# Kernel optimization log

Measured on AMD Instinct MI355X. Metric: run time of the kernel, lower is better.

Reference implementation:

```python
import jax, jax.numpy as jnp
import numpy as np

B, N, M, E, H = 8, 4096, 4, 512, 8
HEAD_DIM = E // H
LN_EPS = 1e-5


def setup_inputs() -> dict:
    key = jax.random.key(0)
    ks = jax.random.split(key, 12)
    inp = {}
    for i in range(M):
        inp[f"f{i}"] = jax.random.normal(ks[i], (B, N, E), dtype=jnp.float32)
    # learned query (flattened from [1,1,E])
    inp["q_param"] = jax.random.normal(ks[4], (E,), dtype=jnp.float32)
    # torch nn.MultiheadAttention packed in-projection [3E, E] and bias [3E]
    inp["in_proj_w"] = jax.random.normal(ks[5], (3 * E, E), dtype=jnp.float32) * 0.02
    inp["in_proj_b"] = jnp.zeros((3 * E,), dtype=jnp.float32)
    inp["out_proj_w"] = jax.random.normal(ks[6], (E, E), dtype=jnp.float32) * 0.02
    inp["out_proj_b"] = jnp.zeros((E,), dtype=jnp.float32)
    inp["ln_gamma"] = jnp.ones((E,), dtype=jnp.float32)
    inp["ln_beta"] = jnp.zeros((E,), dtype=jnp.float32)
    return inp


def reference(f0, f1, f2, f3, q_param, in_proj_w, in_proj_b, out_proj_w, out_proj_b, ln_gamma, ln_beta):
    x = jnp.stack([f0, f1, f2, f3], axis=2)  # [B, N, M, E]
    b, n, m, e = x.shape
    h, d = H, e // H
    scale = 1.0 / np.sqrt(d)

    Wq, Wk, Wv = jnp.split(in_proj_w, 3, axis=0)  # each [E, E]
    bq, bk, bv = jnp.split(in_proj_b, 3)

    # single learned query, shared across all (b, n) instances
    qh = ((Wq @ q_param + bq) * scale).reshape(h, d)  # [H, d]

    k = (jnp.einsum('bnme,fe->bnmf', x, Wk) + bk).reshape(b, n, m, h, d)
    v = (jnp.einsum('bnme,fe->bnmf', x, Wv) + bv).reshape(b, n, m, h, d)

    scores = jnp.einsum('hd,bnmhd->bnhm', qh, k)        # [B, N, H, M]
    attn = jax.nn.softmax(scores, axis=-1)
    o = jnp.einsum('bnhm,bnmhd->bnhd', attn, v).reshape(b, n, e)
    o = o @ out_proj_w.T + out_proj_b                   # [B, N, E]

    mu = jnp.mean(o, axis=-1, keepdims=True)
    var = jnp.var(o, axis=-1, keepdims=True)
    return (o - mu) * jax.lax.rsqrt(var + LN_EPS) * ln_gamma + ln_beta
```

## Files before the change

### kernel.cpp

```cpp
#include <hip/hip_runtime.h>
#include <hip/hip_bf16.h>


typedef float  f32x4  __attribute__((ext_vector_type(4)));
typedef float  f32x16 __attribute__((ext_vector_type(16)));
typedef short  short8 __attribute__((ext_vector_type(8)));

typedef __attribute__((address_space(1))) const void GV;
typedef __attribute__((address_space(3))) void LV;

__device__ __forceinline__ unsigned short f2bf(float f) {
  unsigned int x = __float_as_uint(f);
  unsigned int r = (x + 0x7fffu + ((x >> 16) & 1u)) >> 16;
  return (unsigned short)r;
}

__device__ __forceinline__ short8 pack8(const f32x4& a, const f32x4& b) {
  unsigned int r0, r1, r2, r3;
  asm("v_cvt_pk_bf16_f32 %0, %1, %2" : "=v"(r0) : "v"(a[0]), "v"(a[1]));
  asm("v_cvt_pk_bf16_f32 %0, %1, %2" : "=v"(r1) : "v"(a[2]), "v"(a[3]));
  asm("v_cvt_pk_bf16_f32 %0, %1, %2" : "=v"(r2) : "v"(b[0]), "v"(b[1]));
  asm("v_cvt_pk_bf16_f32 %0, %1, %2" : "=v"(r3) : "v"(b[2]), "v"(b[3]));
  short8 r;
  r[0] = (short)(r0 & 0xffff); r[1] = (short)(r0 >> 16);
  r[2] = (short)(r1 & 0xffff); r[3] = (short)(r1 >> 16);
  r[4] = (short)(r2 & 0xffff); r[5] = (short)(r2 >> 16);
  r[6] = (short)(r3 & 0xffff); r[7] = (short)(r3 >> 16);
  return r;
}

__device__ __forceinline__ void mfma32(f32x16& c, short8 a, short8 b) {
  asm("v_mfma_f32_32x32x16_bf16 %0, %1, %2, %0" : "+v"(c) : "v"(a), "v"(b));
}
__device__ __forceinline__ void mfma16(f32x4& c, short8 a, short8 b) {
  asm("v_mfma_f32_16x16x32_bf16 %0, %1, %2, %0" : "+v"(c) : "v"(a), "v"(b));
}

__device__ __forceinline__ void gld4s(short8& d, const unsigned short* p) {
  asm volatile("global_load_dwordx4 %0, %1, off" : "=v"(d) : "v"(p));
}

#define WAITV(n) asm volatile("s_waitcnt vmcnt(" #n ")" ::: "memory")

__device__ __forceinline__ void wbv12(short8& a, short8& b, short8& c, short8& d,
                                      short8& e, short8& f, short8& g, short8& h) {
  asm volatile("s_waitcnt vmcnt(12)"
               : "+v"(a), "+v"(b), "+v"(c), "+v"(d),
                 "+v"(e), "+v"(f), "+v"(g), "+v"(h));
}
__device__ __forceinline__ void wbv8(short8& a, short8& b, short8& c, short8& d,
                                     short8& e, short8& f, short8& g, short8& h) {
  asm volatile("s_waitcnt vmcnt(8)"
               : "+v"(a), "+v"(b), "+v"(c), "+v"(d),
                 "+v"(e), "+v"(f), "+v"(g), "+v"(h));
}
__device__ __forceinline__ void wbv0(short8& a, short8& b, short8& c, short8& d,
                                     short8& e, short8& f, short8& g, short8& h) {
  asm volatile("s_waitcnt vmcnt(0)"
               : "+v"(a), "+v"(b), "+v"(c), "+v"(d),
                 "+v"(e), "+v"(f), "+v"(g), "+v"(h));
}

__global__ void __launch_bounds__(512) tdcp_k0(
    const float* __restrict__ q_param, const float* __restrict__ in_w,
    const float* __restrict__ in_b, const float* __restrict__ out_w,
    float* __restrict__ scoreb, unsigned short* __restrict__ wscB,
    unsigned short* __restrict__ WvB, unsigned short* __restrict__ WoB)
{
  const int tid = threadIdx.x;
  const int blk = blockIdx.x;
  if (blk < 8) {
    const int h = blk;
    __shared__ float qls[512];
    __shared__ float qs[64];
    qls[tid] = q_param[tid];
    __syncthreads();
    {
      const int io = tid >> 3, sub = tid & 7;
      const float* wrow = in_w + (size_t)(h * 64 + io) * 512;
      float v = 0.f;
      #pragma unroll 8
      for (int ee = 0; ee < 64; ++ee) {
        const int e = sub + (ee << 3);
        v += wrow[e] * qls[e];
      }
      v += __shfl_xor(v, 1); v += __shfl_xor(v, 2); v += __shfl_xor(v, 4);
      if (sub == 0) qs[io] = (v + in_b[h * 64 + io]) * 0.125f;
    }
    __syncthreads();
    {
      const int e = tid;
      const float* wk = in_w + (size_t)(512 + h * 64) * 512 + e;
      float v = 0.f;
      #pragma unroll 8
      for (int jj = 0; jj < 64; ++jj) v += qs[jj] * wk[jj * 512];
      const int s32 = e >> 5, g = (e & 31) >> 3, j = e & 7;
      wscB[((s32 << 6) + h + (g << 4)) * 8 + j] = f2bf(v);
      wscB[((s32 << 6) + (h + 8) + (g << 4)) * 8 + j] = 0;
    }
    if (tid < 64) {
      float v = qs[tid] * in_b[512 + h * 64 + tid];
      v += __shfl_xor(v, 1);  v += __shfl_xor(v, 2);  v += __shfl_xor(v, 4);
      v += __shfl_xor(v, 8);  v += __shfl_xor(v, 16); v += __shfl_xor(v, 32);
      if (tid == 0) scoreb[h] = v;
    }
    if (blk == 0 && tid >= 64 && tid < 72) scoreb[tid - 56] = 0.f;
  } else {
    const int mb = blk - 8;
    const bool isWo = mb >= 64;
    const float* src = isWo ? out_w : (in_w + (size_t)1024 * 512);
    unsigned short* dst = isWo ? WoB : WvB;
    const int slot = ((mb & 63) << 9) + tid;
    const int ct = slot >> 11, kt = (slot >> 6) & 31, ln = slot & 63;
    const float* p = src + (size_t)(ct * 32 + (ln & 31)) * 512
                         + kt * 16 + ((ln >> 5) << 3);
    const f32x4 u0 = *(const f32x4*)(p);
    const f32x4 u1 = *(const f32x4*)(p + 4);
    short8 rr;
    rr[0] = (short)f2bf(u0[0]); rr[1] = (short)f2bf(u0[1]);
    rr[2] = (short)f2bf(u0[2]); rr[3] = (short)f2bf(u0[3]);
    rr[4] = (short)f2bf(u1[0]); rr[5] = (short)f2bf(u1[1]);
    rr[6] = (short)f2bf(u1[2]); rr[7] = (short)f2bf(u1[3]);
    *(short8*)(dst + slot * 8) = rr;
  }
}

__global__ void __launch_bounds__(512, 2) tdcp_k1(
    const float* __restrict__ f0, const float* __restrict__ f1,
    const float* __restrict__ f2, const float* __restrict__ f3,
    const float* __restrict__ in_b,
    const float* __restrict__ scoreb, const unsigned short* __restrict__ wscB,
    const unsigned short* __restrict__ WvB, const unsigned short* __restrict__ WoB,
    const float* __restrict__ out_b, const float* __restrict__ gamma,
    const float* __restrict__ beta, float* __restrict__ out)
{
  extern __shared__ __align__(16) char smem[];
  const int tid = threadIdx.x;
  const int w = tid >> 6;
  const int l = tid & 63;
  const int tok0 = blockIdx.x << 5;

  {
    const f32x4* wsrc = (const f32x4*)wscB;
    f32x4* wdst = (f32x4*)(smem + 98304);
    wdst[tid * 2] = wsrc[tid * 2];
    wdst[tid * 2 + 1] = wsrc[tid * 2 + 1];
  }

  const float* gsrc[4];
  #pragma unroll
  for (int q = 0; q < 4; ++q) {
    const int R = 16 * w + 4 * q + (l >> 4);
    const int m = R & 3, tok = R >> 2;
    const int u = (((l & 15) >> 1) ^ (R & 7));
    gsrc[q] = (m == 0 ? f0 : m == 1 ? f1 : m == 2 ? f2 : f3)
              + (size_t)(tok0 + tok) * 512 + (u << 3) + ((l & 1) << 2);
  }
  const int dmaDst = (w << 12);

  const int aB = (l & 31) << 8;
  int offA[4];
  #pragma unroll
  for (int kt4 = 0; kt4 < 4; ++kt4)
    offA[kt4] = (((2 * kt4 + (l >> 5)) ^ (l & 7)) << 5);
  const int sB = (16 * w + (l & 15)) << 8;
  int offS[2];
  #pragma unroll
  for (int sc = 0; sc < 2; ++sc)
    offS[sc] = (((4 * sc + (l >> 4)) ^ (l & 7)) << 5);

  const int ct0 = w << 1;
  const unsigned short* wv0 = WvB + (((ct0 * 32) << 6) + l) * 8;
  const unsigned short* wv1 = WvB + ((((ct0 + 1) * 32) << 6) + l) * 8;
  const unsigned short* wscL = (const unsigned short*)(smem + 98304);

  f32x16 acc[4][2];
  f32x4 sacc;
  #pragma unroll
  for (int i = 0; i < 4; ++i)
    #pragma unroll
    for (int cc = 0; cc < 2; ++cc)
      #pragma unroll
      for (int r = 0; r < 16; ++r) acc[i][cc][r] = 0.f;
  sacc[0] = sacc[1] = sacc[2] = sacc[3] = 0.f;

  short8 bb[2][8];

#define DMA(S) do { \
    char* db_ = smem + 32768 * ((S) % 3) + dmaDst; \
    __builtin_amdgcn_global_load_lds((GV*)(gsrc[0] + (S) * 64), (LV*)(db_),        16, 0, 0); \
    __builtin_amdgcn_global_load_lds((GV*)(gsrc[1] + (S) * 64), (LV*)(db_ + 1024), 16, 0, 0); \
    __builtin_amdgcn_global_load_lds((GV*)(gsrc[2] + (S) * 64), (LV*)(db_ + 2048), 16, 0, 0); \
    __builtin_amdgcn_global_load_lds((GV*)(gsrc[3] + (S) * 64), (LV*)(db_ + 3072), 16, 0, 0); \
  } while (0)

#define ISSUE_B(S, bank) do { \
    gld4s(bb[bank][0], wv0 + ((S) * 4 + 0) * 512); \
    gld4s(bb[bank][1], wv1 + ((S) * 4 + 0) * 512); \
    gld4s(bb[bank][2], wv0 + ((S) * 4 + 1) * 512); \
    gld4s(bb[bank][3], wv1 + ((S) * 4 + 1) * 512); \
    gld4s(bb[bank][4], wv0 + ((S) * 4 + 2) * 512); \
    gld4s(bb[bank][5], wv1 + ((S) * 4 + 2) * 512); \
    gld4s(bb[bank][6], wv0 + ((S) * 4 + 3) * 512); \
    gld4s(bb[bank][7], wv1 + ((S) * 4 + 3) * 512); \
  } while (0)

  DMA(0); DMA(1);
  ISSUE_B(0, 0);
  WAITV(12);
  asm volatile("s_waitcnt lgkmcnt(0)" ::: "memory");
  __builtin_amdgcn_s_barrier();
  asm volatile("" ::: "memory");

  #pragma unroll
  for (int s = 0; s < 8; ++s) {
    if (s < 6) DMA(s + 2);
    if (s < 7) ISSUE_B(s + 1, (s + 1) & 1);

    short8 (&b)[8] = bb[s & 1];
    if (s < 6)      wbv12(b[0], b[1], b[2], b[3], b[4], b[5], b[6], b[7]);
    else if (s == 6) wbv8(b[0], b[1], b[2], b[3], b[4], b[5], b[6], b[7]);
    else             wbv0(b[0], b[1], b[2], b[3], b[4], b[5], b[6], b[7]);

    const char* cur = smem + 32768 * (s % 3);
    const short8 sb0 = *(const short8*)(wscL + (((2 * s) << 6) + l) * 8);
    const short8 sb1 = *(const short8*)(wscL + (((2 * s + 1) << 6) + l) * 8);
    #pragma unroll
    for (int kt4 = 0; kt4 < 4; ++kt4) {
      #pragma unroll
      for (int rt = 0; rt < 4; ++rt) {
        const char* p = cur + (rt << 13) + aB + offA[kt4];
        const f32x4 lo = *(const f32x4*)(p);
        const f32x4 hi = *(const f32x4*)(p + 16);
        const short8 a = pack8(lo, hi);
        mfma32(acc[rt][0], a, b[kt4 * 2]);
        mfma32(acc[rt][1], a, b[kt4 * 2 + 1]);
      }
      if ((kt4 & 1) == 0) {
        const int sc = kt4 >> 1;
        const char* p = cur + sB + offS[sc];
        const f32x4 lo = *(const f32x4*)(p);
        const f32x4 hi = *(const f32x4*)(p + 16);
        mfma16(sacc, pack8(lo, hi), (sc == 0) ? sb0 : sb1);
      }
    }

    if (s < 6)      { WAITV(12); }
    else if (s == 6) { WAITV(8); }
    if (s < 7) {
      asm volatile("s_waitcnt lgkmcnt(0)" ::: "memory");
      __builtin_amdgcn_s_barrier();
      asm volatile("" ::: "memory");
    }
  }
  asm volatile("s_nop 7\n\ts_nop 7\n\ts_nop 7" ::);

  {
    const int hh = l & 15;
    if (hh < 8) {
      const float sb = scoreb[hh];
      const float s0 = sacc[0] + sb, s1 = sacc[1] + sb;
      const float s2 = sacc[2] + sb, s3 = sacc[3] + sb;
      const float mx = fmaxf(fmaxf(s0, s1), fmaxf(s2, s3));
      const float e0 = __expf(s0 - mx), e1 = __expf(s1 - mx);
      const float e2 = __expf(s2 - mx), e3 = __expf(s3 - mx);
      const float inv = 1.f / (e0 + e1 + e2 + e3);
      f32x4 av; av[0] = e0 * inv; av[1] = e1 * inv; av[2] = e2 * inv; av[3] = e3 * inv;
      const int t = (w << 2) + (l >> 4);
      *(f32x4*)(smem + 65536 + (((t << 3) + hh) << 4)) = av;
    }
  }
  __syncthreads();

  {
    unsigned short* omid = (unsigned short*)(smem);
    #pragma unroll
    for (int c2 = 0; c2 < 2; ++c2) {
      const int ff = ((ct0 + c2) << 5) + (l & 31);
      const float bvf = in_b[1024 + ff];
      const int ktf = ff >> 4;
      const int laneL = ((l >> 3) & 1) << 5;
      const int elem = ff & 7;
      #pragma unroll
      for (int rt = 0; rt < 4; ++rt) {
        #pragma unroll
        for (int tt = 0; tt < 4; ++tt) {
          const int t = (rt << 3) + (tt << 1) + (l >> 5);
          const f32x4 av = *(const f32x4*)(smem + 65536 + (((t << 3) + w) << 4));
          const float o = av[0] * acc[rt][c2][tt * 4 + 0]
                        + av[1] * acc[rt][c2][tt * 4 + 1]
                        + av[2] * acc[rt][c2][tt * 4 + 2]
                        + av[3] * acc[rt][c2][tt * 4 + 3] + bvf;
          omid[((ktf << 6) + t + laneL) * 8 + elem] = f2bf(o);
        }
      }
    }
  }
  __syncthreads();

  f32x16 oa0, oa1;
  #pragma unroll
  for (int r = 0; r < 16; ++r) { oa0[r] = 0.f; oa1[r] = 0.f; }
  const unsigned short* wo0 = WoB + (((ct0 * 32) << 6) + l) * 8;
  const unsigned short* wo1 = WoB + ((((ct0 + 1) * 32) << 6) + l) * 8;
  const int a_off = l << 4;
  #pragma unroll 4
  for (int kt = 0; kt < 32; ++kt) {
    const short8 a = *(const short8*)(smem + (kt << 10) + a_off);
    mfma32(oa0, a, *(const short8*)(wo0 + kt * 512));
    mfma32(oa1, a, *(const short8*)(wo1 + kt * 512));
  }
  asm volatile("s_nop 7\n\ts_nop 7\n\ts_nop 7" ::);

  {
    const int g0 = (ct0 << 5) + (l & 31);
    const int g1 = g0 + 32;
    const float ob0 = out_b[g0], ob1 = out_b[g1];
    const float gm0 = gamma[g0], gm1 = gamma[g1];
    const float bt0 = beta[g0],  bt1 = beta[g1];
    float* stats = (float*)(smem + 69632);
    #pragma unroll
    for (int r = 0; r < 16; ++r) {
      const float v0 = oa0[r] + ob0, v1 = oa1[r] + ob1;
      float s = v0 + v1, qq = v0 * v0 + v1 * v1;
      s += __shfl_xor(s, 16); qq += __shfl_xor(qq, 16);
      s += __shfl_xor(s, 8);  qq += __shfl_xor(qq, 8);
      s += __shfl_xor(s, 4);  qq += __shfl_xor(qq, 4);
      s += __shfl_xor(s, 2);  qq += __shfl_xor(qq, 2);
      s += __shfl_xor(s, 1);  qq += __shfl_xor(qq, 1);
      if ((l & 31) == 0) {
        const int t = (r & 3) + ((r >> 2) << 3) + ((l >> 5) << 2);
        stats[(t << 4) + (w << 1)] = s;
        stats[(t << 4) + (w << 1) + 1] = qq;
      }
    }
    __syncthreads();
    #pragma unroll
    for (int r = 0; r < 16; ++r) {
      const int t = (r & 3) + ((r >> 2) << 3) + ((l >> 5) << 2);
      const float* st = stats + (t << 4);
      float s = 0.f, qq = 0.f;
      #pragma unroll
      for (int ww = 0; ww < 8; ++ww) { s += st[2 * ww]; qq += st[2 * ww + 1]; }
      const float mu = s * 0.001953125f;
      const float rs = rsqrtf(qq * 0.001953125f - mu * mu + 1e-5f);
      const float v0 = oa0[r] + ob0, v1 = oa1[r] + ob1;
      float* op = out + (size_t)(tok0 + t) * 512;
      op[g0] = (v0 - mu) * rs * gm0 + bt0;
      op[g1] = (v1 - mu) * rs * gm1 + bt1;
    }
  }
#undef DMA
#undef ISSUE_B
}

extern "C" void kernel_launch(void* const* d_in, const int* in_sizes, int n_in,
                              void* d_out, int out_size, void* d_ws, size_t ws_size,
                              hipStream_t stream) {
  const float* f0      = (const float*)d_in[0];
  const float* f1      = (const float*)d_in[1];
  const float* f2      = (const float*)d_in[2];
  const float* f3      = (const float*)d_in[3];
  const float* q_param = (const float*)d_in[4];
  const float* in_w    = (const float*)d_in[5];
  const float* in_b    = (const float*)d_in[6];
  const float* out_w   = (const float*)d_in[7];
  const float* out_b   = (const float*)d_in[8];
  const float* gamma   = (const float*)d_in[9];
  const float* beta    = (const float*)d_in[10];
  float* out = (float*)d_out;

  char* ws = (char*)d_ws;
  float* scoreb          = (float*)ws;
  unsigned short* wscB   = (unsigned short*)(ws + 4096);
  unsigned short* WvB    = (unsigned short*)(ws + 20480);
  unsigned short* WoB    = (unsigned short*)(ws + 544768);

  hipFuncSetAttribute((const void*)tdcp_k1,
                      hipFuncAttributeMaxDynamicSharedMemorySize, 114688);

  tdcp_k0<<<136, 512, 0, stream>>>(q_param, in_w, in_b, out_w,
                                   scoreb, wscB, WvB, WoB);
  tdcp_k1<<<1024, 512, 114688, stream>>>(f0, f1, f2, f3, in_b,
                                         scoreb, wscB, WvB, WoB,
                                         out_b, gamma, beta, out);
}
```

Baseline: 154.2 us.

## Switch to double-buffered 64KB LDS stages with half as many barriers

Replaces the triple-buffered 32KB-per-stage DMA pipeline with a double-buffered scheme. Each iteration loads two 32KB sub-stages (64KB) and computes them back to back, with Wv fragment loads interleaved per sub-stage. This halves the number of block-wide barriers and lgkm waits in the main loop while keeping a similar amount of data in flight. It raises dynamic LDS to 144KB and moves the softmax and stats scratch regions, which still allows only one block per CU and changes the vmcnt wait depths.

```diff
diff --git a/kernel.cpp b/kernel.cpp
--- a/kernel.cpp
+++ b/kernel.cpp
@@ -42,9 +42,9 @@
 
 #define WAITV(n) asm volatile("s_waitcnt vmcnt(" #n ")" ::: "memory")
 
-__device__ __forceinline__ void wbv12(short8& a, short8& b, short8& c, short8& d,
+__device__ __forceinline__ void wbv16(short8& a, short8& b, short8& c, short8& d,
                                       short8& e, short8& f, short8& g, short8& h) {
-  asm volatile("s_waitcnt vmcnt(12)"
+  asm volatile("s_waitcnt vmcnt(16)"
                : "+v"(a), "+v"(b), "+v"(c), "+v"(d),
                  "+v"(e), "+v"(f), "+v"(g), "+v"(h));
 }
@@ -142,7 +142,7 @@
 
   {
     const f32x4* wsrc = (const f32x4*)wscB;
-    f32x4* wdst = (f32x4*)(smem + 98304);
+    f32x4* wdst = (f32x4*)(smem + 131072);
     wdst[tid * 2] = wsrc[tid * 2];
     wdst[tid * 2 + 1] = wsrc[tid * 2 + 1];
   }
@@ -172,7 +172,7 @@
   const int ct0 = w << 1;
   const unsigned short* wv0 = WvB + (((ct0 * 32) << 6) + l) * 8;
   const unsigned short* wv1 = WvB + ((((ct0 + 1) * 32) << 6) + l) * 8;
-  const unsigned short* wscL = (const unsigned short*)(smem + 98304);
+  const unsigned short* wscL = (const unsigned short*)(smem + 131072);
 
   f32x16 acc[4][2];
   f32x4 sacc;
@@ -186,68 +186,85 @@
 
   short8 bb[2][8];
 
-#define DMA(S) do { \
-    char* db_ = smem + 32768 * ((S) % 3) + dmaDst; \
-    __builtin_amdgcn_global_load_lds((GV*)(gsrc[0] + (S) * 64), (LV*)(db_),        16, 0, 0); \
-    __builtin_amdgcn_global_load_lds((GV*)(gsrc[1] + (S) * 64), (LV*)(db_ + 1024), 16, 0, 0); \
-    __builtin_amdgcn_global_load_lds((GV*)(gsrc[2] + (S) * 64), (LV*)(db_ + 2048), 16, 0, 0); \
-    __builtin_amdgcn_global_load_lds((GV*)(gsrc[3] + (S) * 64), (LV*)(db_ + 3072), 16, 0, 0); \
+#define DMA(SP) do { \
+    char* db_ = smem + 65536 * ((SP) & 1) + dmaDst; \
+    __builtin_amdgcn_global_load_lds((GV*)(gsrc[0] + (2*(SP)) * 64),     (LV*)(db_),                16, 0, 0); \
+    __builtin_amdgcn_global_load_lds((GV*)(gsrc[1] + (2*(SP)) * 64),     (LV*)(db_ + 1024),         16, 0, 0); \
+    __builtin_amdgcn_global_load_lds((GV*)(gsrc[2] + (2*(SP)) * 64),     (LV*)(db_ + 2048),         16, 0, 0); \
+    __builtin_amdgcn_global_load_lds((GV*)(gsrc[3] + (2*(SP)) * 64),     (LV*)(db_ + 3072),         16, 0, 0); \
+    __builtin_amdgcn_global_load_lds((GV*)(gsrc[0] + (2*(SP)+1) * 64),   (LV*)(db_ + 32768),        16, 0, 0); \
+    __builtin_amdgcn_global_load_lds((GV*)(gsrc[1] + (2*(SP)+1) * 64),   (LV*)(db_ + 32768 + 1024), 16, 0, 0); \
+    __builtin_amdgcn_global_load_lds((GV*)(gsrc[2] + (2*(SP)+1) * 64),   (LV*)(db_ + 32768 + 2048), 16, 0, 0); \
+    __builtin_amdgcn_global_load_lds((GV*)(gsrc[3] + (2*(SP)+1) * 64),   (LV*)(db_ + 32768 + 3072), 16, 0, 0); \
   } while (0)
 
-#define ISSUE_B(S, bank) do { \
-    gld4s(bb[bank][0], wv0 + ((S) * 4 + 0) * 512); \
-    gld4s(bb[bank][1], wv1 + ((S) * 4 + 0) * 512); \
-    gld4s(bb[bank][2], wv0 + ((S) * 4 + 1) * 512); \
-    gld4s(bb[bank][3], wv1 + ((S) * 4 + 1) * 512); \
-    gld4s(bb[bank][4], wv0 + ((S) * 4 + 2) * 512); \
-    gld4s(bb[bank][5], wv1 + ((S) * 4 + 2) * 512); \
-    gld4s(bb[bank][6], wv0 + ((S) * 4 + 3) * 512); \
-    gld4s(bb[bank][7], wv1 + ((S) * 4 + 3) * 512); \
+#define ISSUE_B(G, k) do { \
+    gld4s(bb[k][0], wv0 + ((G) * 4 + 0) * 512); \
+    gld4s(bb[k][1], wv1 + ((G) * 4 + 0) * 512); \
+    gld4s(bb[k][2], wv0 + ((G) * 4 + 1) * 512); \
+    gld4s(bb[k][3], wv1 + ((G) * 4 + 1) * 512); \
+    gld4s(bb[k][4], wv0 + ((G) * 4 + 2) * 512); \
+    gld4s(bb[k][5], wv1 + ((G) * 4 + 2) * 512); \
+    gld4s(bb[k][6], wv0 + ((G) * 4 + 3) * 512); \
+    gld4s(bb[k][7], wv1 + ((G) * 4 + 3) * 512); \
   } while (0)
 
-  DMA(0); DMA(1);
+#define COMPUTE_EG(curE, k, G) do { \
+    const short8 sb0_ = *(const short8*)(wscL + (((2*(G)) << 6) + l) * 8); \
+    const short8 sb1_ = *(const short8*)(wscL + (((2*(G)+1) << 6) + l) * 8); \
+    _Pragma("unroll") \
+    for (int kt4 = 0; kt4 < 4; ++kt4) { \
+      _Pragma("unroll") \
+      for (int rt = 0; rt < 4; ++rt) { \
+        const char* p_ = (curE) + (rt << 13) + aB + offA[kt4]; \
+        const f32x4 lo_ = *(const f32x4*)(p_); \
+        const f32x4 hi_ = *(const f32x4*)(p_ + 16); \
+        const short8 a_ = pack8(lo_, hi_); \
+        mfma32(acc[rt][0], a_, bb[k][kt4 * 2]); \
+        mfma32(acc[rt][1], a_, bb[k][kt4 * 2 + 1]); \
+      } \
+      if ((kt4 & 1) == 0) { \
+        const int sc_ = kt4 >> 1; \
+        const char* p_ = (curE) + sB + offS[sc_]; \
+        const f32x4 lo_ = *(const f32x4*)(p_); \
+        const f32x4 hi_ = *(const f32x4*)(p_ + 16); \
+        mfma16(sacc, pack8(lo_, hi_), (sc_ == 0) ? sb0_ : sb1_); \
+      } \
+    } \
+  } while (0)
+
+#define WB16(k) wbv16(bb[k][0], bb[k][1], bb[k][2], bb[k][3], \
+                      bb[k][4], bb[k][5], bb[k][6], bb[k][7])
+#define WB8(k)  wbv8(bb[k][0], bb[k][1], bb[k][2], bb[k][3], \
+                     bb[k][4], bb[k][5], bb[k][6], bb[k][7])
+#define WB0(k)  wbv0(bb[k][0], bb[k][1], bb[k][2], bb[k][3], \
+                     bb[k][4], bb[k][5], bb[k][6], bb[k][7])
+
+  DMA(0);
   ISSUE_B(0, 0);
-  WAITV(12);
+  ISSUE_B(1, 1);
+  WAITV(16);
   asm volatile("s_waitcnt lgkmcnt(0)" ::: "memory");
   __builtin_amdgcn_s_barrier();
   asm volatile("" ::: "memory");
 
   #pragma unroll
-  for (int s = 0; s < 8; ++s) {
-    if (s < 6) DMA(s + 2);
-    if (s < 7) ISSUE_B(s + 1, (s + 1) & 1);
-
-    short8 (&b)[8] = bb[s & 1];
-    if (s < 6)      wbv12(b[0], b[1], b[2], b[3], b[4], b[5], b[6], b[7]);
-    else if (s == 6) wbv8(b[0], b[1], b[2], b[3], b[4], b[5], b[6], b[7]);
-    else             wbv0(b[0], b[1], b[2], b[3], b[4], b[5], b[6], b[7]);
-
-    const char* cur = smem + 32768 * (s % 3);
-    const short8 sb0 = *(const short8*)(wscL + (((2 * s) << 6) + l) * 8);
-    const short8 sb1 = *(const short8*)(wscL + (((2 * s + 1) << 6) + l) * 8);
-    #pragma unroll
-    for (int kt4 = 0; kt4 < 4; ++kt4) {
-      #pragma unroll
-      for (int rt = 0; rt < 4; ++rt) {
-        const char* p = cur + (rt << 13) + aB + offA[kt4];
-        const f32x4 lo = *(const f32x4*)(p);
-        const f32x4 hi = *(const f32x4*)(p + 16);
-        const short8 a = pack8(lo, hi);
-        mfma32(acc[rt][0], a, b[kt4 * 2]);
-        mfma32(acc[rt][1], a, b[kt4 * 2 + 1]);
-      }
-      if ((kt4 & 1) == 0) {
-        const int sc = kt4 >> 1;
-        const char* p = cur + sB + offS[sc];
-        const f32x4 lo = *(const f32x4*)(p);
-        const f32x4 hi = *(const f32x4*)(p + 16);
-        mfma16(sacc, pack8(lo, hi), (sc == 0) ? sb0 : sb1);
-      }
-    }
-
-    if (s < 6)      { WAITV(12); }
-    else if (s == 6) { WAITV(8); }
-    if (s < 7) {
+  for (int s = 0; s < 4; ++s) {
+    if (s < 3) DMA(s + 1);
+    char* buf = smem + 65536 * (s & 1);
+
+    if (s < 3) WB16(0);
+    else       WB8(0);
+    COMPUTE_EG(buf, 0, 4 * s + 0 - 2 * s);
+    if (s < 3) ISSUE_B(2 * (s + 1), 0);
+
+    if (s < 3) WB16(1);
+    else       WB0(1);
+    COMPUTE_EG(buf + 32768, 1, 2 * s + 1);
+    if (s < 3) ISSUE_B(2 * (s + 1) + 1, 1);
+
+    if (s < 3) {
+      WAITV(16);
       asm volatile("s_waitcnt lgkmcnt(0)" ::: "memory");
       __builtin_amdgcn_s_barrier();
       asm volatile("" ::: "memory");
@@ -267,7 +284,7 @@
       const float inv = 1.f / (e0 + e1 + e2 + e3);
       f32x4 av; av[0] = e0 * inv; av[1] = e1 * inv; av[2] = e2 * inv; av[3] = e3 * inv;
       const int t = (w << 2) + (l >> 4);
-      *(f32x4*)(smem + 65536 + (((t << 3) + hh) << 4)) = av;
+      *(f32x4*)(smem + 32768 + (((t << 3) + hh) << 4)) = av;
     }
   }
   __syncthreads();
@@ -286,7 +303,7 @@
         #pragma unroll
         for (int tt = 0; tt < 4; ++tt) {
           const int t = (rt << 3) + (tt << 1) + (l >> 5);
-          const f32x4 av = *(const f32x4*)(smem + 65536 + (((t << 3) + w) << 4));
+          const f32x4 av = *(const f32x4*)(smem + 32768 + (((t << 3) + w) << 4));
           const float o = av[0] * acc[rt][c2][tt * 4 + 0]
                         + av[1] * acc[rt][c2][tt * 4 + 1]
                         + av[2] * acc[rt][c2][tt * 4 + 2]
@@ -318,7 +335,7 @@
     const float ob0 = out_b[g0], ob1 = out_b[g1];
     const float gm0 = gamma[g0], gm1 = gamma[g1];
     const float bt0 = beta[g0],  bt1 = beta[g1];
-    float* stats = (float*)(smem + 69632);
+    float* stats = (float*)(smem + 36864);
     #pragma unroll
     for (int r = 0; r < 16; ++r) {
       const float v0 = oa0[r] + ob0, v1 = oa1[r] + ob1;
@@ -352,6 +369,10 @@
   }
 #undef DMA
 #undef ISSUE_B
+#undef COMPUTE_EG
+#undef WB16
+#undef WB8
+#undef WB0
 }
 
 extern "C" void kernel_launch(void* const* d_in, const int* in_sizes, int n_in,
@@ -377,11 +398,11 @@
   unsigned short* WoB    = (unsigned short*)(ws + 544768);
 
   hipFuncSetAttribute((const void*)tdcp_k1,
-                      hipFuncAttributeMaxDynamicSharedMemorySize, 114688);
+                      hipFuncAttributeMaxDynamicSharedMemorySize, 147456);
 
   tdcp_k0<<<136, 512, 0, stream>>>(q_param, in_w, in_b, out_w,
                                    scoreb, wscB, WvB, WoB);
-  tdcp_k1<<<1024, 512, 114688, stream>>>(f0, f1, f2, f3, in_b,
+  tdcp_k1<<<1024, 512, 147456, stream>>>(f0, f1, f2, f3, in_b,
                                          scoreb, wscB, WvB, WoB,
                                          out_b, gamma, beta, out);
 }
```

After: 151.2 us. No clear change (-1.9%).
